# Kernel tuning notes

Measured on AMD Instinct MI355X. Metric: run time of the kernel, lower is better.

Reference implementation:

```python
import jax, jax.numpy as jnp
import numpy as np

B, N, DIN, H, D = 16, 1024, 128, 4, 32  # batch, n_agents, input_dim, heads, head_dim
NEG = -9e15


def setup_inputs() -> dict:
    key = jax.random.key(0)
    k1, k2, k3, k4 = jax.random.split(key, 4)
    x = jax.random.normal(k1, (B, N, DIN), jnp.float32)
    adj = jax.random.randint(k2, (B, N, N), 0, 2, jnp.int32)
    # params (xavier-ish scale)
    W = jax.random.normal(k3, (DIN, H * D), jnp.float32) * np.float32(1.0 / np.sqrt(DIN))
    b = jnp.zeros((H * D,), jnp.float32)
    a = jax.random.normal(k4, (2 * D, 1), jnp.float32) * np.float32(0.1)
    return {"x": x, "adj": adj, "W": W, "b": b, "a": a}


def reference(x, adj, W, b, a):
    Bb, Nn, _ = x.shape
    h = (x @ W + b).reshape(Bb, Nn, H, D)              # [B,N,H,D]
    # GAT trick: concat([h_i,h_j]) @ a == h_i@a[:D] + h_j@a[D:]
    a_i, a_j = a[:D, 0], a[D:, 0]
    e_i = jnp.einsum('bnhd,d->bnh', h, a_i)
    e_j = jnp.einsum('bnhd,d->bnh', h, a_j)
    e = e_i[:, :, None, :] + e_j[:, None, :, :]        # [B,N,N,H]
    e = jnp.where(e > 0, e, 0.2 * e)                   # LeakyReLU(0.2)
    e = jnp.where(adj[..., None] > 0, e, NEG)          # adjacency mask
    attn = jax.nn.softmax(e, axis=2)                   # softmax over neighbors j
    out = jnp.einsum('bijh,bjhd->bihd', attn, h)       # per-head aggregation
    return out.reshape(Bb, Nn, H * D)                  # concat heads
```

## Files before the change

kernel.cpp:

```cpp
#include <hip/hip_runtime.h>
#include <hip/hip_bf16.h>

#define Bdim 16
#define Ndim 1024
#define DINc 128
#define Hh   4
#define Dd   32
#define HDc  128
#define L2E  1.4426950408889634f

typedef float  float4v  __attribute__((ext_vector_type(4)));
typedef int    int4v    __attribute__((ext_vector_type(4)));
typedef short  short8   __attribute__((ext_vector_type(8)));
typedef unsigned short ushort4v __attribute__((ext_vector_type(4)));

__device__ __forceinline__ unsigned short bf16_rne(float f) {
    unsigned u = __float_as_uint(f);
    u = u + 0x7FFFu + ((u >> 16) & 1u);
    return (unsigned short)(u >> 16);
}

__device__ __forceinline__ void gl_lds16(const void* g, void* l) {
    __builtin_amdgcn_global_load_lds(
        (const __attribute__((address_space(1))) unsigned int*)g,
        (__attribute__((address_space(3))) unsigned int*)l, 16, 0, 0);
}

__global__ __launch_bounds__(256) void pack_kernel(
    const int* __restrict__ adj, unsigned long long* __restrict__ pk64)
{
    const int g = (blockIdx.x * 256 + threadIdx.x) >> 6;
    const int lane = threadIdx.x & 63;
    const int* src = adj + (size_t)g * 2048 + lane;
    #pragma unroll 4
    for (int k = 0; k < 32; ++k) {
        int v = src[k * 64];
        unsigned long long m = __ballot(v > 0);
        if (lane == 0) pk64[(size_t)g * 32 + k] = m;
    }
}

__global__ __launch_bounds__(256) void split_w_kernel(
    const float* __restrict__ W, const float* __restrict__ bias,
    const float* __restrict__ a,
    unsigned short* __restrict__ WTh, unsigned short* __restrict__ WTl,
    float* __restrict__ bias2)
{
    const int t = threadIdx.x, blk = blockIdx.x;
    if (blk < 16) {
        int r  = blk * 8 + (t >> 5);
        int k0 = (t & 31) * 4;
        #pragma unroll
        for (int j = 0; j < 4; ++j) {
            float f = W[(size_t)(k0 + j) * HDc + r];
            unsigned short hi = bf16_rne(f);
            WTh[r * 128 + k0 + j] = hi;
            WTl[r * 128 + k0 + j] = bf16_rne(f - __uint_as_float((unsigned)hi << 16));
        }
    } else {
        #pragma unroll
        for (int rep = 0; rep < 2; ++rep) {
            int task = t + rep * 256;
            int row = task >> 2, hh = task & 3;
            float si = 0.f, sj = 0.f;
            #pragma unroll
            for (int d4 = 0; d4 < 8; ++d4) {
                float4v wv = *(const float4v*)(W + (size_t)row * HDc + hh * 32 + d4 * 4);
                float4v av = *(const float4v*)(a + d4 * 4);
                float4v bv = *(const float4v*)(a + Dd + d4 * 4);
                #pragma unroll
                for (int kk = 0; kk < 4; ++kk) {
                    si = fmaf(wv[kk], av[kk], si);
                    sj = fmaf(wv[kk], bv[kk], sj);
                }
            }
            float vi = si * L2E, vj = sj * L2E;
            unsigned short hi = bf16_rne(vi);
            WTh[(128 + hh) * 128 + row] = hi;
            WTl[(128 + hh) * 128 + row] = bf16_rne(vi - __uint_as_float((unsigned)hi << 16));
            unsigned short hj = bf16_rne(vj);
            WTh[(132 + hh) * 128 + row] = hj;
            WTl[(132 + hh) * 128 + row] = bf16_rne(vj - __uint_as_float((unsigned)hj << 16));
        }
        #pragma unroll
        for (int rp = 0; rp < 4; ++rp) {
            int idx = t + rp * 256;
            WTh[136 * 128 + idx] = 0;
            WTl[136 * 128 + idx] = 0;
        }
        if (t < 128) {
            bias2[t] = bias[t];
        } else if (t < 136) {
            int z = t - 128;
            const float* av = (z < 4) ? a : a + Dd;
            int hh = z & 3;
            float s = 0.f;
            for (int d = 0; d < 32; ++d) s = fmaf(bias[hh * 32 + d], av[d], s);
            bias2[128 + z] = s * L2E;
        } else if (t < 144) {
            bias2[t] = 0.f;
        }
    }
}

__global__ __launch_bounds__(256) void proj_kernel(
    const float* __restrict__ x,
    const unsigned short* __restrict__ WTh, const unsigned short* __restrict__ WTl,
    const float* __restrict__ bias2,
    unsigned short* __restrict__ hTh, unsigned short* __restrict__ hTl,
    float* __restrict__ eiT, float* __restrict__ ejT)
{
    __shared__ unsigned char xs[4][8192];
    const int t = threadIdx.x, lane = t & 63, w = t >> 6;
    const int tile = blockIdx.x * 4 + w;
    const int nb = tile * 16;
    const int b = nb >> 10, nloc = nb & 1023;
    const int l16 = lane & 15, q = lane >> 4;

    {
        const char* gx = (const char*)(x + (size_t)nb * DINc);
        char* lx = (char*)xs[w];
        int rsub = lane >> 5;
        int p = lane & 31;
        #pragma unroll
        for (int c = 0; c < 8; ++c) {
            int ra = c * 2 + rsub;
            int gb = (p & 24) | ((p & 7) ^ (ra & 7));
            gl_lds16(gx + (size_t)ra * 512 + gb * 16, lx + c * 1024);
        }
    }
    asm volatile("s_waitcnt vmcnt(0)" ::: "memory");

    float4v C[9];
    #pragma unroll
    for (int nt = 0; nt < 9; ++nt) C[nt] = (float4v){0.f, 0.f, 0.f, 0.f};

    const int sw = l16 & 7;
    #pragma unroll
    for (int ks = 0; ks < 4; ++ks) {
        int blk0 = ks * 8 + 2 * q;
        int p0 = (blk0 & 24) | ((blk0 & 7) ^ sw);
        int p1 = ((blk0 + 1) & 24) | (((blk0 + 1) & 7) ^ sw);
        float4v x0 = *(const float4v*)(xs[w] + l16 * 512 + p0 * 16);
        float4v x1 = *(const float4v*)(xs[w] + l16 * 512 + p1 * 16);
        short8 Ah, Al;
        #pragma unroll
        for (int e = 0; e < 8; ++e) {
            float f = (e < 4) ? x0[e] : x1[e - 4];
            unsigned short hi = bf16_rne(f);
            Ah[e] = (short)hi;
            Al[e] = (short)bf16_rne(f - __uint_as_float((unsigned)hi << 16));
        }
        #pragma unroll
        for (int nt = 0; nt < 9; ++nt) {
            size_t wo = (size_t)(nt * 16 + l16) * 128 + ks * 32 + q * 8;
            short8 Bh = *(const short8*)(WTh + wo);
            short8 Bl = *(const short8*)(WTl + wo);
            C[nt] = __builtin_amdgcn_mfma_f32_16x16x32_bf16(Ah, Bh, C[nt], 0, 0, 0);
            C[nt] = __builtin_amdgcn_mfma_f32_16x16x32_bf16(Ah, Bl, C[nt], 0, 0, 0);
            C[nt] = __builtin_amdgcn_mfma_f32_16x16x32_bf16(Al, Bh, C[nt], 0, 0, 0);
        }
    }

    const int nodeloc = nloc + q * 4;
    #pragma unroll
    for (int nt = 0; nt < 8; ++nt) {
        int col = nt * 16 + l16;
        float bv = bias2[col];
        ushort4v h4, l4;
        #pragma unroll
        for (int r = 0; r < 4; ++r) {
            float f = C[nt][r] + bv;
            unsigned short hs = bf16_rne(f);
            h4[r] = hs;
            l4[r] = bf16_rne(f - __uint_as_float((unsigned)hs << 16));
        }
        size_t off = (size_t)(b * HDc + col) * Ndim + nodeloc;
        *(ushort4v*)(hTh + off) = h4;
        *(ushort4v*)(hTl + off) = l4;
    }
    {
        float bv = bias2[128 + l16];
        float4v v = {C[8][0] + bv, C[8][1] + bv, C[8][2] + bv, C[8][3] + bv};
        if (l16 < 4)
            *(float4v*)(eiT + (size_t)(b * Hh + l16) * Ndim + nodeloc) = v;
        else if (l16 < 8)
            *(float4v*)(ejT + (size_t)(b * Hh + (l16 - 4)) * Ndim + nodeloc) = v;
    }
}

__global__ __launch_bounds__(256) void gat_kernel(
    const unsigned int* __restrict__ pk,
    const unsigned short* __restrict__ hTh, const unsigned short* __restrict__ hTl,
    const float* __restrict__ eiT, const float* __restrict__ ejT,
    float* __restrict__ out)
{
    __shared__ unsigned char smem[73728];
    const int t = threadIdx.x, lane = t & 63, w = t >> 6;
    const int L = blockIdx.x;
    const int b = (L & 7) + 8 * ((L >> 3) & 1);
    const int ibase = (L >> 4) * 64;
    const int i = lane & 15, q = lane >> 4;

    {
        int r = t >> 2, dbase = (t & 3) * 8;
        const unsigned int* src = pk + ((size_t)(b * Ndim + ibase + r)) * 32 + dbase;
        int4v v0 = *(const int4v*)(src);
        int4v v1 = *(const int4v*)(src + 4);
        unsigned int* dst = (unsigned int*)smem + r * 32;
        #pragma unroll
        for (int k = 0; k < 4; ++k) dst[(dbase + k + r) & 31] = (unsigned)v0[k];
        #pragma unroll
        for (int k = 0; k < 4; ++k) dst[(dbase + 4 + k + r) & 31] = (unsigned)v1[k];
    }
    float ei_[4];
    #pragma unroll
    for (int it = 0; it < 4; ++it)
        ei_[it] = eiT[(size_t)(b * Hh + w) * Ndim + ibase + it * 16 + i];

    __syncthreads();

    const char* gej = (const char*)(ejT + ((size_t)b * Hh + w) * Ndim);
    char* lej = (char*)smem + 8192 + w * 4096;
    #pragma unroll
    for (int c = 0; c < 4; ++c)
        gl_lds16(gej + c * 1024 + lane * 16, lej + c * 1024);

    const char* gh  = (const char*)(hTh + ((size_t)b * HDc + w * Dd) * Ndim);
    const char* glo = (const char*)(hTl + ((size_t)b * HDc + w * Dd) * Ndim);
    const int drel = lane >> 2, m = lane & 3;
    const int s = m ^ ((drel >> 1) & 3);
    const size_t lane_off = (size_t)drel * 2048 + s * 16;
    char* lws = (char*)smem + 24576 + w * 12288;

#define ISSUE(JT, SLOT) {                                              \
    const char* gh_ = gh  + (size_t)(JT) * 64;                         \
    const char* gl_ = glo + (size_t)(JT) * 64;                         \
    char* lb_ = lws + (SLOT) * 4096;                                   \
    gl_lds16(gh_ + lane_off,         lb_);                             \
    gl_lds16(gh_ + 32768 + lane_off, lb_ + 1024);                      \
    gl_lds16(gl_ + lane_off,         lb_ + 2048);                      \
    gl_lds16(gl_ + 32768 + lane_off, lb_ + 3072); }

    ISSUE(0, 0); ISSUE(1, 1);

    float4v C[4][2];
    #pragma unroll
    for (int it = 0; it < 4; ++it) {
        C[it][0] = (float4v){0.f, 0.f, 0.f, 0.f};
        C[it][1] = (float4v){0.f, 0.f, 0.f, 0.f};
    }
    float den[4] = {0.f, 0.f, 0.f, 0.f};
    const unsigned int* pkl = (const unsigned int*)smem;
    const float* ejl = (const float*)(smem + 8192 + w * 4096);
    const int xo = ((q ^ ((i >> 1) & 3)) << 4);

    int slot_c = 0;
    for (int jt = 0; jt < 32; ++jt) {
        int ji = jt + 2; if (ji > 31) ji = 31;
        int slot_i = slot_c + 2; if (slot_i >= 3) slot_i -= 3;
        ISSUE(ji, slot_i);
        asm volatile("s_waitcnt vmcnt(8)" ::: "memory");

        const char* lb = lws + slot_c * 4096;
        short8 Bh0 = *(const short8*)(lb + i * 64 + xo);
        short8 Bh1 = *(const short8*)(lb + 1024 + i * 64 + xo);
        short8 Bl0 = *(const short8*)(lb + 2048 + i * 64 + xo);
        short8 Bl1 = *(const short8*)(lb + 3072 + i * 64 + xo);
        float4v e0 = *(const float4v*)(ejl + jt * 32 + q * 8);
        float4v e1 = *(const float4v*)(ejl + jt * 32 + q * 8 + 4);

        #pragma unroll
        for (int it = 0; it < 4; ++it) {
            int r = it * 16 + i;
            unsigned bits = (pkl[r * 32 + ((jt + r) & 31)] >> (q * 8)) & 0xffu;
            float p[8];
            #pragma unroll
            for (int k = 0; k < 8; ++k) {
                float ev = (k < 4) ? e0[k] : e1[k - 4];
                float e = ei_[it] + ev;
                float sL = e > 0.f ? e : 0.2f * e;
                float pe = ((bits >> k) & 1u) ? __builtin_amdgcn_exp2f(sL) : 0.f;
                den[it] += pe;
                p[k] = pe;
            }
            union { __hip_bfloat162 h2[4]; short8 s8; } A;
            #pragma unroll
            for (int k2 = 0; k2 < 4; ++k2)
                A.h2[k2] = __float22bfloat162_rn(make_float2(p[2 * k2], p[2 * k2 + 1]));
            C[it][0] = __builtin_amdgcn_mfma_f32_16x16x32_bf16(A.s8, Bh0, C[it][0], 0, 0, 0);
            C[it][0] = __builtin_amdgcn_mfma_f32_16x16x32_bf16(A.s8, Bl0, C[it][0], 0, 0, 0);
            C[it][1] = __builtin_amdgcn_mfma_f32_16x16x32_bf16(A.s8, Bh1, C[it][1], 0, 0, 0);
            C[it][1] = __builtin_amdgcn_mfma_f32_16x16x32_bf16(A.s8, Bl1, C[it][1], 0, 0, 0);
        }
        slot_c = (slot_c == 2) ? 0 : slot_c + 1;
    }
#undef ISSUE

    #pragma unroll
    for (int it = 0; it < 4; ++it) {
        float d_ = den[it];
        d_ += __shfl_xor(d_, 16);
        d_ += __shfl_xor(d_, 32);
        den[it] = d_;
    }
    float* outp = out + ((size_t)(b * Ndim + ibase)) * HDc + w * Dd + i;
    #pragma unroll
    for (int it = 0; it < 4; ++it) {
        #pragma unroll
        for (int reg = 0; reg < 4; ++reg) {
            int row = it * 16 + q * 4 + reg;
            float rd = 1.0f / __shfl(den[it], q * 4 + reg, 64);
            outp[(size_t)row * HDc]      = C[it][0][reg] * rd;
            outp[(size_t)row * HDc + 16] = C[it][1][reg] * rd;
        }
    }
}

extern "C" void kernel_launch(void* const* d_in, const int* in_sizes, int n_in,
                              void* d_out, int out_size, void* d_ws, size_t ws_size,
                              hipStream_t stream) {
    const float* x    = (const float*)d_in[0];
    const int*   adj  = (const int*)d_in[1];
    const float* W    = (const float*)d_in[2];
    const float* bias = (const float*)d_in[3];
    const float* a    = (const float*)d_in[4];
    float* out = (float*)d_out;

    unsigned long long* pk64 = (unsigned long long*)d_ws;
    unsigned int* pk32 = (unsigned int*)d_ws;
    unsigned short* hTh = (unsigned short*)((char*)d_ws + 2 * 1024 * 1024);
    unsigned short* hTl = hTh + (size_t)Bdim * HDc * Ndim;
    float* eiT = (float*)(hTl + (size_t)Bdim * HDc * Ndim);
    float* ejT = eiT + (size_t)Bdim * Hh * Ndim;
    unsigned short* WTh = (unsigned short*)(ejT + (size_t)Bdim * Hh * Ndim);
    unsigned short* WTl = WTh + 144 * 128;
    float* bias2 = (float*)(WTl + 144 * 128);

    split_w_kernel<<<dim3(17), dim3(256), 0, stream>>>(W, bias, a, WTh, WTl, bias2);
    pack_kernel<<<dim3(2048), dim3(256), 0, stream>>>(adj, pk64);
    proj_kernel<<<dim3(256), dim3(256), 0, stream>>>(
        x, WTh, WTl, bias2, hTh, hTl, eiT, ejT);
    gat_kernel<<<dim3(256), dim3(256), 0, stream>>>(
        pk32, hTh, hTl, eiT, ejT, out);
}
```

Baseline: 172.9 us.

## Fuse adjacency packing into GAT kernel, drop bf16 low half of h, retile projection

Removes the separate pack kernel and packs the int32 adjacency into bitmasks inside the attention kernel with ballots and nontemporal loads. It also drops the low-order bf16 half of h, which halves the h traffic and the MFMA count. The attention tile shrinks to 32 rows so twice as many blocks run. The projection kernel now stages W into LDS and processes 128 nodes per block. Storing h in a single bf16 reduces accuracy of the aggregation, and adj is now read directly by the kernel that also computes.

```diff
diff --git a/kernel.cpp b/kernel.cpp
--- a/kernel.cpp
+++ b/kernel.cpp
@@ -3,14 +3,11 @@
 
 #define Bdim 16
 #define Ndim 1024
-#define DINc 128
 #define Hh   4
-#define Dd   32
 #define HDc  128
 #define L2E  1.4426950408889634f
 
 typedef float  float4v  __attribute__((ext_vector_type(4)));
-typedef int    int4v    __attribute__((ext_vector_type(4)));
 typedef short  short8   __attribute__((ext_vector_type(8)));
 typedef unsigned short ushort4v __attribute__((ext_vector_type(4)));
 
@@ -24,20 +21,6 @@
     __builtin_amdgcn_global_load_lds(
         (const __attribute__((address_space(1))) unsigned int*)g,
         (__attribute__((address_space(3))) unsigned int*)l, 16, 0, 0);
-}
-
-__global__ __launch_bounds__(256) void pack_kernel(
-    const int* __restrict__ adj, unsigned long long* __restrict__ pk64)
-{
-    const int g = (blockIdx.x * 256 + threadIdx.x) >> 6;
-    const int lane = threadIdx.x & 63;
-    const int* src = adj + (size_t)g * 2048 + lane;
-    #pragma unroll 4
-    for (int k = 0; k < 32; ++k) {
-        int v = src[k * 64];
-        unsigned long long m = __ballot(v > 0);
-        if (lane == 0) pk64[(size_t)g * 32 + k] = m;
-    }
 }
 
 __global__ __launch_bounds__(256) void split_w_kernel(
@@ -67,7 +50,7 @@
             for (int d4 = 0; d4 < 8; ++d4) {
                 float4v wv = *(const float4v*)(W + (size_t)row * HDc + hh * 32 + d4 * 4);
                 float4v av = *(const float4v*)(a + d4 * 4);
-                float4v bv = *(const float4v*)(a + Dd + d4 * 4);
+                float4v bv = *(const float4v*)(a + 32 + d4 * 4);
                 #pragma unroll
                 for (int kk = 0; kk < 4; ++kk) {
                     si = fmaf(wv[kk], av[kk], si);
@@ -92,7 +75,7 @@
             bias2[t] = bias[t];
         } else if (t < 136) {
             int z = t - 128;
-            const float* av = (z < 4) ? a : a + Dd;
+            const float* av = (z < 4) ? a : a + 32;
             int hh = z & 3;
             float s = 0.f;
             for (int d = 0; d < 32; ++d) s = fmaf(bias[hh * 32 + d], av[d], s);
@@ -103,183 +86,193 @@
     }
 }
 
-__global__ __launch_bounds__(256) void proj_kernel(
+__global__ __launch_bounds__(256, 1) void proj_kernel(
     const float* __restrict__ x,
-    const unsigned short* __restrict__ WTh, const unsigned short* __restrict__ WTl,
+    const unsigned short* __restrict__ WTg_h, const unsigned short* __restrict__ WTg_l,
     const float* __restrict__ bias2,
-    unsigned short* __restrict__ hTh, unsigned short* __restrict__ hTl,
-    float* __restrict__ eiT, float* __restrict__ ejT)
+    unsigned short* __restrict__ hTh, float* __restrict__ eiT, float* __restrict__ ejT)
 {
-    __shared__ unsigned char xs[4][8192];
+    __shared__ unsigned char smem[139264];
+    char* xls  = (char*)smem;
+    char* wtls = (char*)smem + 65536;
+
     const int t = threadIdx.x, lane = t & 63, w = t >> 6;
-    const int tile = blockIdx.x * 4 + w;
-    const int nb = tile * 16;
+    const int l16 = lane & 15, q = lane >> 4;
+    const int nb = blockIdx.x * 128;
     const int b = nb >> 10, nloc = nb & 1023;
-    const int l16 = lane & 15, q = lane >> 4;
 
     {
-        const char* gx = (const char*)(x + (size_t)nb * DINc);
-        char* lx = (char*)xs[w];
-        int rsub = lane >> 5;
-        int p = lane & 31;
-        #pragma unroll
-        for (int c = 0; c < 8; ++c) {
-            int ra = c * 2 + rsub;
-            int gb = (p & 24) | ((p & 7) ^ (ra & 7));
-            gl_lds16(gx + (size_t)ra * 512 + gb * 16, lx + c * 1024);
-        }
-    }
-    asm volatile("s_waitcnt vmcnt(0)" ::: "memory");
-
-    float4v C[9];
-    #pragma unroll
-    for (int nt = 0; nt < 9; ++nt) C[nt] = (float4v){0.f, 0.f, 0.f, 0.f};
-
-    const int sw = l16 & 7;
+        const char* gx = (const char*)(x + (size_t)nb * 128);
+        int rh = lane >> 5, m = lane & 31;
+        #pragma unroll
+        for (int d = 0; d < 16; ++d) {
+            int r = w * 32 + d * 2 + rh;
+            int mg = m ^ (r & 7);
+            gl_lds16(gx + (size_t)r * 512 + mg * 16, xls + (size_t)w * 16384 + d * 1024);
+        }
+    }
+    {
+        int rh = lane >> 4, m = lane & 15;
+        #pragma unroll
+        for (int d = 0; d < 18; ++d) {
+            int n = w * 18 + d;
+            if (n < 36) {
+                int r = n * 4 + rh;
+                gl_lds16((const char*)WTg_h + (size_t)r * 256 + (m ^ (r & 15)) * 16,
+                         wtls + (size_t)n * 1024);
+            } else {
+                int r = (n - 36) * 4 + rh;
+                gl_lds16((const char*)WTg_l + (size_t)r * 256 + (m ^ (r & 15)) * 16,
+                         wtls + (size_t)n * 1024);
+            }
+        }
+    }
+    __syncthreads();
+
+    float4v C[2][9];
+    #pragma unroll
+    for (int g = 0; g < 2; ++g)
+        #pragma unroll
+        for (int nt = 0; nt < 9; ++nt) C[g][nt] = (float4v){0.f, 0.f, 0.f, 0.f};
+
     #pragma unroll
     for (int ks = 0; ks < 4; ++ks) {
-        int blk0 = ks * 8 + 2 * q;
-        int p0 = (blk0 & 24) | ((blk0 & 7) ^ sw);
-        int p1 = ((blk0 + 1) & 24) | (((blk0 + 1) & 7) ^ sw);
-        float4v x0 = *(const float4v*)(xs[w] + l16 * 512 + p0 * 16);
-        float4v x1 = *(const float4v*)(xs[w] + l16 * 512 + p1 * 16);
-        short8 Ah, Al;
-        #pragma unroll
-        for (int e = 0; e < 8; ++e) {
-            float f = (e < 4) ? x0[e] : x1[e - 4];
-            unsigned short hi = bf16_rne(f);
-            Ah[e] = (short)hi;
-            Al[e] = (short)bf16_rne(f - __uint_as_float((unsigned)hi << 16));
+        short8 Ah[2], Al[2];
+        #pragma unroll
+        for (int g = 0; g < 2; ++g) {
+            int r = w * 32 + g * 16 + l16;
+            int c0 = (ks * 8 + q * 2) ^ (l16 & 7);
+            int c1 = (ks * 8 + q * 2 + 1) ^ (l16 & 7);
+            float4v x0 = *(const float4v*)(xls + (size_t)r * 512 + c0 * 16);
+            float4v x1 = *(const float4v*)(xls + (size_t)r * 512 + c1 * 16);
+            #pragma unroll
+            for (int e = 0; e < 8; ++e) {
+                float f = (e < 4) ? x0[e] : x1[e - 4];
+                unsigned short hi = bf16_rne(f);
+                Ah[g][e] = (short)hi;
+                Al[g][e] = (short)bf16_rne(f - __uint_as_float((unsigned)hi << 16));
+            }
         }
         #pragma unroll
         for (int nt = 0; nt < 9; ++nt) {
-            size_t wo = (size_t)(nt * 16 + l16) * 128 + ks * 32 + q * 8;
-            short8 Bh = *(const short8*)(WTh + wo);
-            short8 Bl = *(const short8*)(WTl + wo);
-            C[nt] = __builtin_amdgcn_mfma_f32_16x16x32_bf16(Ah, Bh, C[nt], 0, 0, 0);
-            C[nt] = __builtin_amdgcn_mfma_f32_16x16x32_bf16(Ah, Bl, C[nt], 0, 0, 0);
-            C[nt] = __builtin_amdgcn_mfma_f32_16x16x32_bf16(Al, Bh, C[nt], 0, 0, 0);
-        }
-    }
-
-    const int nodeloc = nloc + q * 4;
-    #pragma unroll
-    for (int nt = 0; nt < 8; ++nt) {
-        int col = nt * 16 + l16;
-        float bv = bias2[col];
-        ushort4v h4, l4;
-        #pragma unroll
-        for (int r = 0; r < 4; ++r) {
-            float f = C[nt][r] + bv;
-            unsigned short hs = bf16_rne(f);
-            h4[r] = hs;
-            l4[r] = bf16_rne(f - __uint_as_float((unsigned)hs << 16));
-        }
-        size_t off = (size_t)(b * HDc + col) * Ndim + nodeloc;
-        *(ushort4v*)(hTh + off) = h4;
-        *(ushort4v*)(hTl + off) = l4;
-    }
-    {
+            const char* wb = wtls + (size_t)(nt * 16 + l16) * 256 + ((ks * 4 + q) ^ l16) * 16;
+            short8 Bh = *(const short8*)wb;
+            short8 Bl = *(const short8*)(wb + 36864);
+            #pragma unroll
+            for (int g = 0; g < 2; ++g) {
+                C[g][nt] = __builtin_amdgcn_mfma_f32_16x16x32_bf16(Ah[g], Bh, C[g][nt], 0, 0, 0);
+                C[g][nt] = __builtin_amdgcn_mfma_f32_16x16x32_bf16(Ah[g], Bl, C[g][nt], 0, 0, 0);
+                C[g][nt] = __builtin_amdgcn_mfma_f32_16x16x32_bf16(Al[g], Bh, C[g][nt], 0, 0, 0);
+            }
+        }
+    }
+
+    #pragma unroll
+    for (int g = 0; g < 2; ++g) {
+        int node = nloc + w * 32 + g * 16 + q * 4;
+        #pragma unroll
+        for (int nt = 0; nt < 8; ++nt) {
+            int col = nt * 16 + l16;
+            float bv = bias2[col];
+            ushort4v h4;
+            #pragma unroll
+            for (int r = 0; r < 4; ++r) h4[r] = bf16_rne(C[g][nt][r] + bv);
+            *(ushort4v*)(hTh + (size_t)(b * HDc + col) * Ndim + node) = h4;
+        }
         float bv = bias2[128 + l16];
-        float4v v = {C[8][0] + bv, C[8][1] + bv, C[8][2] + bv, C[8][3] + bv};
+        float4v v = {C[g][8][0] + bv, C[g][8][1] + bv, C[g][8][2] + bv, C[g][8][3] + bv};
         if (l16 < 4)
-            *(float4v*)(eiT + (size_t)(b * Hh + l16) * Ndim + nodeloc) = v;
+            *(float4v*)(eiT + (size_t)(b * Hh + l16) * Ndim + node) = v;
         else if (l16 < 8)
-            *(float4v*)(ejT + (size_t)(b * Hh + (l16 - 4)) * Ndim + nodeloc) = v;
-    }
-}
-
-__global__ __launch_bounds__(256) void gat_kernel(
-    const unsigned int* __restrict__ pk,
-    const unsigned short* __restrict__ hTh, const unsigned short* __restrict__ hTl,
+            *(float4v*)(ejT + (size_t)(b * Hh + (l16 - 4)) * Ndim + node) = v;
+    }
+}
+
+__global__ __launch_bounds__(256, 2) void gat_kernel(
+    const int* __restrict__ adj, const unsigned short* __restrict__ hTh,
     const float* __restrict__ eiT, const float* __restrict__ ejT,
     float* __restrict__ out)
 {
-    __shared__ unsigned char smem[73728];
+    __shared__ unsigned char smem[45056];
+    unsigned int* pkl = (unsigned int*)smem;
+    float* ejl = (float*)(smem + 4096);
+    char* rings = (char*)smem + 20480;
+
     const int t = threadIdx.x, lane = t & 63, w = t >> 6;
     const int L = blockIdx.x;
     const int b = (L & 7) + 8 * ((L >> 3) & 1);
-    const int ibase = (L >> 4) * 64;
+    const int ibase = (L >> 4) * 32;
     const int i = lane & 15, q = lane >> 4;
 
     {
-        int r = t >> 2, dbase = (t & 3) * 8;
-        const unsigned int* src = pk + ((size_t)(b * Ndim + ibase + r)) * 32 + dbase;
-        int4v v0 = *(const int4v*)(src);
-        int4v v1 = *(const int4v*)(src + 4);
-        unsigned int* dst = (unsigned int*)smem + r * 32;
-        #pragma unroll
-        for (int k = 0; k < 4; ++k) dst[(dbase + k + r) & 31] = (unsigned)v0[k];
-        #pragma unroll
-        for (int k = 0; k < 4; ++k) dst[(dbase + 4 + k + r) & 31] = (unsigned)v1[k];
-    }
-    float ei_[4];
-    #pragma unroll
-    for (int it = 0; it < 4; ++it)
-        ei_[it] = eiT[(size_t)(b * Hh + w) * Ndim + ibase + it * 16 + i];
-
+        const int* arow = adj + ((size_t)(b * Ndim + ibase + w * 8)) * Ndim + lane;
+        #pragma unroll
+        for (int rl = 0; rl < 8; ++rl) {
+            int r = w * 8 + rl;
+            #pragma unroll
+            for (int c = 0; c < 16; ++c) {
+                int v = __builtin_nontemporal_load(arow + (size_t)rl * Ndim + c * 64);
+                unsigned long long m = __ballot(v > 0);
+                if (lane == 0)  pkl[r * 32 + ((2 * c + r) & 31)]     = (unsigned)m;
+                if (lane == 32) pkl[r * 32 + ((2 * c + 1 + r) & 31)] = (unsigned)(m >> 32);
+            }
+        }
+    }
+    const float ei0 = eiT[(size_t)(b * Hh + w) * Ndim + ibase + i];
+    const float ei1 = eiT[(size_t)(b * Hh + w) * Ndim + ibase + 16 + i];
     __syncthreads();
 
-    const char* gej = (const char*)(ejT + ((size_t)b * Hh + w) * Ndim);
-    char* lej = (char*)smem + 8192 + w * 4096;
-    #pragma unroll
-    for (int c = 0; c < 4; ++c)
-        gl_lds16(gej + c * 1024 + lane * 16, lej + c * 1024);
-
-    const char* gh  = (const char*)(hTh + ((size_t)b * HDc + w * Dd) * Ndim);
-    const char* glo = (const char*)(hTl + ((size_t)b * HDc + w * Dd) * Ndim);
-    const int drel = lane >> 2, m = lane & 3;
-    const int s = m ^ ((drel >> 1) & 3);
-    const size_t lane_off = (size_t)drel * 2048 + s * 16;
-    char* lws = (char*)smem + 24576 + w * 12288;
-
-#define ISSUE(JT, SLOT) {                                              \
-    const char* gh_ = gh  + (size_t)(JT) * 64;                         \
-    const char* gl_ = glo + (size_t)(JT) * 64;                         \
-    char* lb_ = lws + (SLOT) * 4096;                                   \
-    gl_lds16(gh_ + lane_off,         lb_);                             \
-    gl_lds16(gh_ + 32768 + lane_off, lb_ + 1024);                      \
-    gl_lds16(gl_ + lane_off,         lb_ + 2048);                      \
-    gl_lds16(gl_ + 32768 + lane_off, lb_ + 3072); }
+    {
+        const char* gej = (const char*)(ejT + (size_t)(b * Hh + w) * Ndim);
+        #pragma unroll
+        for (int c = 0; c < 4; ++c)
+            gl_lds16(gej + c * 1024 + lane * 16, (char*)(ejl + w * 1024) + c * 1024);
+    }
+
+    const char* gh = (const char*)(hTh + (size_t)(b * HDc + w * 32) * Ndim);
+    const size_t lane_g = (size_t)(lane >> 2) * 2048 + (lane & 3) * 16;
+    char* ringw = rings + w * 6144;
+
+#define ISSUE(JT, SLOT) {                                                   \
+    char* lb_ = ringw + (SLOT) * 2048;                                      \
+    gl_lds16(gh + (size_t)(JT) * 64 + lane_g,         lb_);                 \
+    gl_lds16(gh + 32768 + (size_t)(JT) * 64 + lane_g, lb_ + 1024); }
 
     ISSUE(0, 0); ISSUE(1, 1);
 
-    float4v C[4][2];
-    #pragma unroll
-    for (int it = 0; it < 4; ++it) {
-        C[it][0] = (float4v){0.f, 0.f, 0.f, 0.f};
-        C[it][1] = (float4v){0.f, 0.f, 0.f, 0.f};
-    }
-    float den[4] = {0.f, 0.f, 0.f, 0.f};
-    const unsigned int* pkl = (const unsigned int*)smem;
-    const float* ejl = (const float*)(smem + 8192 + w * 4096);
-    const int xo = ((q ^ ((i >> 1) & 3)) << 4);
+    float4v C0[2], C1[2];
+    #pragma unroll
+    for (int it = 0; it < 2; ++it) {
+        C0[it] = (float4v){0.f, 0.f, 0.f, 0.f};
+        C1[it] = (float4v){0.f, 0.f, 0.f, 0.f};
+    }
+    float den[2] = {0.f, 0.f};
+    const float* ejw = ejl + w * 1024;
 
     int slot_c = 0;
     for (int jt = 0; jt < 32; ++jt) {
         int ji = jt + 2; if (ji > 31) ji = 31;
         int slot_i = slot_c + 2; if (slot_i >= 3) slot_i -= 3;
         ISSUE(ji, slot_i);
-        asm volatile("s_waitcnt vmcnt(8)" ::: "memory");
-
-        const char* lb = lws + slot_c * 4096;
-        short8 Bh0 = *(const short8*)(lb + i * 64 + xo);
-        short8 Bh1 = *(const short8*)(lb + 1024 + i * 64 + xo);
-        short8 Bl0 = *(const short8*)(lb + 2048 + i * 64 + xo);
-        short8 Bl1 = *(const short8*)(lb + 3072 + i * 64 + xo);
-        float4v e0 = *(const float4v*)(ejl + jt * 32 + q * 8);
-        float4v e1 = *(const float4v*)(ejl + jt * 32 + q * 8 + 4);
-
-        #pragma unroll
-        for (int it = 0; it < 4; ++it) {
+        asm volatile("s_waitcnt vmcnt(4)" ::: "memory");
+
+        const char* lb = ringw + slot_c * 2048;
+        short8 Bh0 = *(const short8*)(lb + i * 64 + q * 16);
+        short8 Bh1 = *(const short8*)(lb + 1024 + i * 64 + q * 16);
+        float4v e0 = *(const float4v*)(ejw + jt * 32 + q * 8);
+        float4v e1 = *(const float4v*)(ejw + jt * 32 + q * 8 + 4);
+
+        #pragma unroll
+        for (int it = 0; it < 2; ++it) {
             int r = it * 16 + i;
             unsigned bits = (pkl[r * 32 + ((jt + r) & 31)] >> (q * 8)) & 0xffu;
+            float my_ei = it ? ei1 : ei0;
             float p[8];
             #pragma unroll
             for (int k = 0; k < 8; ++k) {
                 float ev = (k < 4) ? e0[k] : e1[k - 4];
-                float e = ei_[it] + ev;
-                float sL = e > 0.f ? e : 0.2f * e;
+                float e = my_ei + ev;
+                float sL = fmaxf(e, 0.2f * e);
                 float pe = ((bits >> k) & 1u) ? __builtin_amdgcn_exp2f(sL) : 0.f;
                 den[it] += pe;
                 p[k] = pe;
@@ -288,31 +281,29 @@
             #pragma unroll
             for (int k2 = 0; k2 < 4; ++k2)
                 A.h2[k2] = __float22bfloat162_rn(make_float2(p[2 * k2], p[2 * k2 + 1]));
-            C[it][0] = __builtin_amdgcn_mfma_f32_16x16x32_bf16(A.s8, Bh0, C[it][0], 0, 0, 0);
-            C[it][0] = __builtin_amdgcn_mfma_f32_16x16x32_bf16(A.s8, Bl0, C[it][0], 0, 0, 0);
-            C[it][1] = __builtin_amdgcn_mfma_f32_16x16x32_bf16(A.s8, Bh1, C[it][1], 0, 0, 0);
-            C[it][1] = __builtin_amdgcn_mfma_f32_16x16x32_bf16(A.s8, Bl1, C[it][1], 0, 0, 0);
+            C0[it] = __builtin_amdgcn_mfma_f32_16x16x32_bf16(A.s8, Bh0, C0[it], 0, 0, 0);
+            C1[it] = __builtin_amdgcn_mfma_f32_16x16x32_bf16(A.s8, Bh1, C1[it], 0, 0, 0);
         }
         slot_c = (slot_c == 2) ? 0 : slot_c + 1;
     }
 #undef ISSUE
 
     #pragma unroll
-    for (int it = 0; it < 4; ++it) {
+    for (int it = 0; it < 2; ++it) {
         float d_ = den[it];
         d_ += __shfl_xor(d_, 16);
         d_ += __shfl_xor(d_, 32);
         den[it] = d_;
     }
-    float* outp = out + ((size_t)(b * Ndim + ibase)) * HDc + w * Dd + i;
-    #pragma unroll
-    for (int it = 0; it < 4; ++it) {
+    float* outp = out + ((size_t)(b * Ndim + ibase)) * HDc + w * 32 + i;
+    #pragma unroll
+    for (int it = 0; it < 2; ++it) {
         #pragma unroll
         for (int reg = 0; reg < 4; ++reg) {
             int row = it * 16 + q * 4 + reg;
             float rd = 1.0f / __shfl(den[it], q * 4 + reg, 64);
-            outp[(size_t)row * HDc]      = C[it][0][reg] * rd;
-            outp[(size_t)row * HDc + 16] = C[it][1][reg] * rd;
+            outp[(size_t)row * HDc]      = C0[it][reg] * rd;
+            outp[(size_t)row * HDc + 16] = C1[it][reg] * rd;
         }
     }
 }
@@ -327,20 +318,16 @@
     const float* a    = (const float*)d_in[4];
     float* out = (float*)d_out;
 
-    unsigned long long* pk64 = (unsigned long long*)d_ws;
-    unsigned int* pk32 = (unsigned int*)d_ws;
-    unsigned short* hTh = (unsigned short*)((char*)d_ws + 2 * 1024 * 1024);
-    unsigned short* hTl = hTh + (size_t)Bdim * HDc * Ndim;
-    float* eiT = (float*)(hTl + (size_t)Bdim * HDc * Ndim);
+    unsigned short* hTh = (unsigned short*)d_ws;
+    float* eiT = (float*)(hTh + (size_t)Bdim * HDc * Ndim);
     float* ejT = eiT + (size_t)Bdim * Hh * Ndim;
     unsigned short* WTh = (unsigned short*)(ejT + (size_t)Bdim * Hh * Ndim);
     unsigned short* WTl = WTh + 144 * 128;
     float* bias2 = (float*)(WTl + 144 * 128);
 
     split_w_kernel<<<dim3(17), dim3(256), 0, stream>>>(W, bias, a, WTh, WTl, bias2);
-    pack_kernel<<<dim3(2048), dim3(256), 0, stream>>>(adj, pk64);
-    proj_kernel<<<dim3(256), dim3(256), 0, stream>>>(
-        x, WTh, WTl, bias2, hTh, hTl, eiT, ejT);
-    gat_kernel<<<dim3(256), dim3(256), 0, stream>>>(
-        pk32, hTh, hTl, eiT, ejT, out);
-}
+    proj_kernel<<<dim3(128), dim3(256), 0, stream>>>(
+        x, WTh, WTl, bias2, hTh, eiT, ejT);
+    gat_kernel<<<dim3(512), dim3(256), 0, stream>>>(
+        adj, hTh, eiT, ejT, out);
+}
```

After: 197.9 us. 14.5% more time.
